# Performance work log

Hardware: AMD Instinct MI355X
Metric: run time of the kernel (lower is better)

Reference implementation:

```python
import jax, jax.numpy as jnp
import numpy as np

B, T, D_IN, N_UNITS, N_OUT = 128, 2048, 256, 512, 64
EPS, GAMMA = 0.01, 0.01


def setup_inputs() -> dict:
    key = jax.random.key(0)
    ks = jax.random.split(key, 5)
    x = jax.random.normal(ks[0], (B, T, D_IN), dtype=jnp.float32)
    # Linear weights ~ N(0, 1/input_dim) per the torch init
    Vh_w = jax.random.normal(ks[1], (N_UNITS, D_IN), dtype=jnp.float32) / D_IN
    Vh_b = jnp.zeros((N_UNITS,), dtype=jnp.float32)
    Vz_w = jax.random.normal(ks[2], (N_UNITS, D_IN), dtype=jnp.float32) / D_IN
    Vz_b = jnp.zeros((N_UNITS,), dtype=jnp.float32)
    # W ~ N(0, init_W_std/input_dim), square [n_units, n_units]
    W = jax.random.normal(ks[3], (N_UNITS, N_UNITS), dtype=jnp.float32) / D_IN
    fc_w = jax.random.normal(ks[4], (N_OUT, N_UNITS), dtype=jnp.float32) * 0.02
    fc_b = jnp.zeros((N_OUT,), dtype=jnp.float32)
    return {"x": x, "Vh_w": Vh_w, "Vh_b": Vh_b, "Vz_w": Vz_w, "Vz_b": Vz_b,
            "W": W, "fc_w": fc_w, "fc_b": fc_b}


def reference(x, Vh_w, Vh_b, Vz_w, Vz_b, W, fc_w, fc_b):
    n_units = W.shape[0]
    # precompute antisymmetric-minus-diffusion matrix once
    A = W - W.T - GAMMA * jnp.eye(n_units, dtype=W.dtype)
    # precompute input projections for all timesteps (batched GEMM)
    vh_x = jnp.einsum('btd,nd->btn', x, Vh_w) + Vh_b  # [B,T,N]
    vz_x = jnp.einsum('btd,nd->btn', x, Vz_w) + Vz_b  # [B,T,N]

    def step(h, inp):
        vh_t, vz_t = inp
        WmWT_h = h @ A                       # [B,N]
        f = jnp.tanh(WmWT_h + vh_t) * jax.nn.sigmoid(WmWT_h + vz_t)
        h = h + EPS * f
        return h, None

    h0 = jnp.zeros((x.shape[0], n_units), dtype=x.dtype)
    # scan over time: inputs shaped [T,B,N]
    hT, _ = jax.lax.scan(step, h0,
                         (jnp.swapaxes(vh_x, 0, 1), jnp.swapaxes(vz_x, 0, 1)))
    return hT @ fc_w.T + fc_b
```

## Files before the change

### kernel.cpp

```cpp
#include <hip/hip_runtime.h>
#include <stdint.h>

#define B_SZ   128
#define T_LEN  2048
#define DIN    256
#define NU     512
#define NOUT   64
#define EPS_F  0.01f
#define GAM_F  0.01f
#define KT     32
#define NTILES (T_LEN / KT)

typedef uint32_t u32;
typedef _Float16 h16;
typedef _Float16 __attribute__((ext_vector_type(2))) h16x2;
typedef _Float16 __attribute__((ext_vector_type(8))) h16x8;
typedef float    __attribute__((ext_vector_type(4))) f32x4;
typedef unsigned int __attribute__((ext_vector_type(4))) u32x4;

#define WS_A    0
#define WS_WH   131072
#define WS_WZ   196608
#define WS_EXCH 262144
#define NQUAD   43

__device__ __forceinline__ u32 pack2(float lo, float hi) {
  h16x2 v; v.x = (h16)lo; v.y = (h16)hi;
  return __builtin_bit_cast(u32, v);
}

__device__ __forceinline__ float fdot2(u32 h2, u32 a2, float acc) {
#if __has_builtin(__builtin_amdgcn_fdot2)
  return __builtin_amdgcn_fdot2(__builtin_bit_cast(h16x2, h2),
                                __builtin_bit_cast(h16x2, a2), acc, false);
#else
  h16x2 hh = __builtin_bit_cast(h16x2, h2);
  h16x2 aa = __builtin_bit_cast(h16x2, a2);
  return acc + (float)hh.x * (float)aa.x + (float)hh.y * (float)aa.y;
#endif
}

__global__ void antirnn_prep(const float* __restrict__ Vh_w,
                             const float* __restrict__ Vz_w,
                             const float* __restrict__ W,
                             u32* __restrict__ ws,
                             float* __restrict__ out) {
  const int idx = blockIdx.x * blockDim.x + threadIdx.x;
  const int stride = gridDim.x * blockDim.x;

  for (int u = idx; u < 131072; u += stride) {
    int e  = u & 3;
    int l  = (u >> 2) & 63;
    int pq = (u >> 8) & 15;
    int c4 = (u >> 12) & 3;
    int w  = (u >> 14) & 3;
    int jh = (u >> 16) & 1;
    int p  = pq * 4 + e;
    int i0 = w * 128 + 2 * p;
    int j  = jh * 256 + l * 4 + c4;
    float lo = W[i0 * NU + j]       - W[j * NU + i0]     - (i0 == j     ? GAM_F : 0.f);
    float hi = W[(i0 + 1) * NU + j] - W[j * NU + i0 + 1] - ((i0 + 1) == j ? GAM_F : 0.f);
    ws[WS_A + u] = pack2(lo, hi);
  }
  for (int u = idx; u < 65536; u += stride) {
    int fl = u * 2;
    ws[WS_WH + u] = pack2(Vh_w[fl], Vh_w[fl + 1]);
    ws[WS_WZ + u] = pack2(Vz_w[fl], Vz_w[fl + 1]);
  }
  for (int u = idx; u < B_SZ * 2 * 2 * NQUAD * 4; u += stride) ws[WS_EXCH + u] = 0;
  for (int u = idx; u < B_SZ * NOUT; u += stride) out[u] = 0.f;
}

__global__ __launch_bounds__(256, 1) void antirnn_scan(
    const float* __restrict__ x,
    const float* __restrict__ vh_b, const float* __restrict__ vz_b,
    const float* __restrict__ fc_w, const float* __restrict__ fc_b,
    u32* __restrict__ ws, float* __restrict__ out) {

  __shared__ h16  xs[32 * 256];
  __shared__ h16  ph[256 * 36];
  __shared__ h16  pz[256 * 36];
  __shared__ float part[4 * 256];
  __shared__ u32  hp[256];

  const int tid = threadIdx.x;
  const int w   = tid >> 6;
  const int l   = tid & 63;
  const int bid = blockIdx.x;
  const int b   = bid & 127;
  const int jh  = bid >> 7;

  u32 a[256];
  {
    const uint4* Ap = reinterpret_cast<const uint4*>(ws + WS_A) + (jh * 4 + w) * 4096 + l;
#pragma unroll
    for (int rq = 0; rq < 64; ++rq) {
      uint4 q = Ap[rq * 64];
      int base = (rq >> 4) * 64 + (rq & 15) * 4;
      a[base + 0] = q.x; a[base + 1] = q.y; a[base + 2] = q.z; a[base + 3] = q.w;
    }
  }

  hp[tid] = 0;

  const float* xrow = x + (long)b * T_LEN * DIN;
  float hreg = 0.f;
  const h16* Wn_h = reinterpret_cast<const h16*>(ws + WS_WH);
  const h16* Wn_z = reinterpret_cast<const h16*>(ws + WS_WZ);
  uint4* exch = reinterpret_cast<uint4*>(ws + WS_EXCH);

  const int  peerHalf   = 1 - jh;
  const bool isPeerWave = ((w >> 1) == peerHalf);
  const int  qbase      = (w & 1) * 21;

#pragma unroll 1
  for (int tile = 0; tile < NTILES; ++tile) {
#pragma unroll
    for (int it = 0; it < 16; ++it) {
      int fp = it * 256 + tid;
      int s  = fp >> 7, dp = fp & 127;
      float2 v = *reinterpret_cast<const float2*>(xrow + (tile * KT + s) * DIN + dp * 2);
      int byteaddr = (s * 512 + dp * 4) ^ ((s & 7) << 4);
      *reinterpret_cast<u32*>(reinterpret_cast<char*>(xs) + byteaddr) = pack2(v.x, v.y);
    }
    __syncthreads();

    {
      f32x4 acch[2][4], accz[2][4];
#pragma unroll
      for (int mt = 0; mt < 2; ++mt)
#pragma unroll
        for (int nt = 0; nt < 4; ++nt) {
          acch[mt][nt] = (f32x4){0.f, 0.f, 0.f, 0.f};
          accz[mt][nt] = (f32x4){0.f, 0.f, 0.f, 0.f};
        }
      const int lk = (l >> 4) * 8;
      const int ln = l & 15;
#pragma unroll
      for (int kk = 0; kk < 8; ++kk) {
        h16x8 af[2];
#pragma unroll
        for (int mt = 0; mt < 2; ++mt) {
          int s = mt * 16 + ln;
          int byteaddr = (s * 512 + kk * 64 + (l >> 4) * 16) ^ ((s & 7) << 4);
          af[mt] = *reinterpret_cast<const h16x8*>(reinterpret_cast<const char*>(xs) + byteaddr);
        }
#pragma unroll
        for (int nt = 0; nt < 4; ++nt) {
          int ng = jh * 256 + w * 64 + nt * 16 + ln;
          h16x8 bh = *reinterpret_cast<const h16x8*>(Wn_h + ng * 256 + kk * 32 + lk);
          h16x8 bz = *reinterpret_cast<const h16x8*>(Wn_z + ng * 256 + kk * 32 + lk);
#pragma unroll
          for (int mt = 0; mt < 2; ++mt) {
            acch[mt][nt] = __builtin_amdgcn_mfma_f32_16x16x32_f16(af[mt], bh, acch[mt][nt], 0, 0, 0);
            accz[mt][nt] = __builtin_amdgcn_mfma_f32_16x16x32_f16(af[mt], bz, accz[mt][nt], 0, 0, 0);
          }
        }
      }
#pragma unroll
      for (int nt = 0; nt < 4; ++nt) {
        int n  = w * 64 + nt * 16 + ln;
        float bh_ = vh_b[jh * 256 + n];
        float bz_ = vz_b[jh * 256 + n];
#pragma unroll
        for (int mt = 0; mt < 2; ++mt) {
          int s0 = mt * 16 + (l >> 4) * 4;
          *reinterpret_cast<u32*>(&ph[n * 36 + s0])     = pack2(acch[mt][nt].x + bh_, acch[mt][nt].y + bh_);
          *reinterpret_cast<u32*>(&ph[n * 36 + s0 + 2]) = pack2(acch[mt][nt].z + bh_, acch[mt][nt].w + bh_);
          *reinterpret_cast<u32*>(&pz[n * 36 + s0])     = pack2(accz[mt][nt].x + bz_, accz[mt][nt].y + bz_);
          *reinterpret_cast<u32*>(&pz[n * 36 + s0 + 2]) = pack2(accz[mt][nt].z + bz_, accz[mt][nt].w + bz_);
        }
      }
    }
    __syncthreads();

#pragma unroll 1
    for (int s = 0; s < KT; ++s) {
      const int t = tile * KT + s;

      if (isPeerWave && t > 0 && l <= 21) {
        int q = qbase + l;
        const uint4* src = exch + (((b * 2 + peerHalf) * 2 + (t & 1)) * NQUAD) + q;
        u32x4 v;
        do {
          asm volatile("global_load_dwordx4 %0, %1, off sc0 sc1\n\ts_waitcnt vmcnt(0)"
                       : "=v"(v) : "v"(src) : "memory");
        } while (v[0] != (u32)t);
#pragma unroll
        for (int k2 = 0; k2 < 3; ++k2) {
          int pi = q * 3 + k2;
          if (pi < 128) hp[peerHalf * 128 + pi] = v[1 + k2];
        }
      }

      u32 hq[64];
      {
        const uint4* hpw = reinterpret_cast<const uint4*>(&hp[w * 64]);
#pragma unroll
        for (int pq = 0; pq < 16; ++pq) {
          uint4 qq = hpw[pq];
          hq[pq * 4 + 0] = qq.x; hq[pq * 4 + 1] = qq.y;
          hq[pq * 4 + 2] = qq.z; hq[pq * 4 + 3] = qq.w;
        }
      }
      float acc0 = 0.f, acc1 = 0.f, acc2 = 0.f, acc3 = 0.f;
#pragma unroll
      for (int p = 0; p < 64; ++p) {
        acc0 = fdot2(hq[p], a[p],        acc0);
        acc1 = fdot2(hq[p], a[64 + p],   acc1);
        acc2 = fdot2(hq[p], a[128 + p],  acc2);
        acc3 = fdot2(hq[p], a[192 + p],  acc3);
      }
      {
        f32x4 pv = {acc0, acc1, acc2, acc3};
        *reinterpret_cast<f32x4*>(&part[w * 256 + l * 4]) = pv;
      }
      __syncthreads();

      {
        float pre = part[tid] + part[256 + tid] + part[512 + tid] + part[768 + tid];
        float uh  = pre + (float)ph[tid * 36 + s];
        float uz  = pre + (float)pz[tid * 36 + s];
        float uhc = fminf(fmaxf(uh, -20.f), 20.f);
        float e2  = __expf(2.f * uhc);
        float th  = 1.f - 2.f / (e2 + 1.f);
        float sg  = 1.f / (1.f + __expf(-uz));
        hreg += EPS_F * th * sg;
        float other = __shfl_xor(hreg, 1, 64);
        if (!(tid & 1)) hp[jh * 128 + (tid >> 1)] = pack2(hreg, other);
      }
      __syncthreads();

      if ((t + 1 < T_LEN) && w == 0 && l < NQUAD) {
        int p0 = l * 3;
        u32 v0 = hp[jh * 128 + p0];
        u32 v1 = (p0 + 1 < 128) ? hp[jh * 128 + p0 + 1] : 0u;
        u32 v2 = (p0 + 2 < 128) ? hp[jh * 128 + p0 + 2] : 0u;
        u32x4 qd; qd[0] = (u32)(t + 1); qd[1] = v0; qd[2] = v1; qd[3] = v2;
        uint4* dst = exch + (((b * 2 + jh) * 2 + ((t + 1) & 1)) * NQUAD) + l;
        asm volatile("global_store_dwordx4 %0, %1, off sc0 sc1"
                     :: "v"(dst), "v"(qd) : "memory");
      }
    }
  }

  __syncthreads();
  part[tid] = hreg;
  __syncthreads();
  if (tid < NOUT) {
    float acc = (jh == 0) ? fc_b[tid] : 0.f;
    const float* fr = fc_w + tid * NU + jh * 256;
#pragma unroll 4
    for (int c = 0; c < 256; ++c) acc += part[c] * fr[c];
    atomicAdd(out + b * NOUT + tid, acc);
  }
}

extern "C" void kernel_launch(void* const* d_in, const int* in_sizes, int n_in,
                              void* d_out, int out_size, void* d_ws, size_t ws_size,
                              hipStream_t stream) {
  const float* x    = (const float*)d_in[0];
  const float* Vh_w = (const float*)d_in[1];
  const float* Vh_b = (const float*)d_in[2];
  const float* Vz_w = (const float*)d_in[3];
  const float* Vz_b = (const float*)d_in[4];
  const float* W    = (const float*)d_in[5];
  const float* fc_w = (const float*)d_in[6];
  const float* fc_b = (const float*)d_in[7];
  float* out = (float*)d_out;
  u32*   ws  = (u32*)d_ws;

  antirnn_prep<<<512, 256, 0, stream>>>(Vh_w, Vz_w, W, ws, out);
  antirnn_scan<<<256, 256, 0, stream>>>(x, Vh_b, Vz_b, fc_w, fc_b, ws, out);
}
```

Baseline: 4.993 ms.

## Interleave two batch chains per block to hide cross-block exchange latency

Each block now handles two batch rows and alternates their recurrence steps, so one chain's peer exchange can be in flight while the other chain computes. Peer h-state for the next chain is prefetched asynchronously into LDS with global_load_lds, and the code falls back to polling only if the flag is stale. The grid drops from 256 to 128 blocks. Per-block serial work doubles and only half the CUs are used, in exchange for hiding the inter-block synchronisation latency that dominates each step.

```diff
diff --git a/kernel.cpp b/kernel.cpp
--- a/kernel.cpp
+++ b/kernel.cpp
@@ -10,6 +10,7 @@
 #define GAM_F  0.01f
 #define KT     32
 #define NTILES (T_LEN / KT)
+#define NC     2
 
 typedef uint32_t u32;
 typedef _Float16 h16;
@@ -17,6 +18,9 @@
 typedef _Float16 __attribute__((ext_vector_type(8))) h16x8;
 typedef float    __attribute__((ext_vector_type(4))) f32x4;
 typedef unsigned int __attribute__((ext_vector_type(4))) u32x4;
+
+typedef const __attribute__((address_space(1))) u32* gas_u32p;
+typedef __attribute__((address_space(3))) u32* las_u32p;
 
 #define WS_A    0
 #define WS_WH   131072
@@ -78,17 +82,19 @@
     u32* __restrict__ ws, float* __restrict__ out) {
 
   __shared__ h16  xs[32 * 256];
-  __shared__ h16  ph[256 * 36];
-  __shared__ h16  pz[256 * 36];
+  __shared__ h16  ph[NC][256 * 36];
+  __shared__ h16  pz[NC][256 * 36];
   __shared__ float part[4 * 256];
-  __shared__ u32  hp[256];
+  __shared__ u32  hp[NC * 256];
+  __shared__ u32x4 stageQ[NC][44];
 
   const int tid = threadIdx.x;
   const int w   = tid >> 6;
   const int l   = tid & 63;
   const int bid = blockIdx.x;
-  const int b   = bid & 127;
-  const int jh  = bid >> 7;
+  const int g   = bid & 63;
+  const int jh  = bid >> 6;
+  const int b0  = g * NC;
 
   u32 a[256];
   {
@@ -101,158 +107,187 @@
     }
   }
 
-  hp[tid] = 0;
-
-  const float* xrow = x + (long)b * T_LEN * DIN;
-  float hreg = 0.f;
+  hp[tid] = 0; hp[256 + tid] = 0;
+
+  float hreg[NC] = {0.f, 0.f};
   const h16* Wn_h = reinterpret_cast<const h16*>(ws + WS_WH);
   const h16* Wn_z = reinterpret_cast<const h16*>(ws + WS_WZ);
   uint4* exch = reinterpret_cast<uint4*>(ws + WS_EXCH);
 
   const int  peerHalf   = 1 - jh;
   const bool isPeerWave = ((w >> 1) == peerHalf);
-  const int  qbase      = (w & 1) * 21;
+  const int  wl         = w & 1;
+  const int  qbase      = wl * 21;
+  const int  sendWave   = jh * 2;
 
 #pragma unroll 1
   for (int tile = 0; tile < NTILES; ++tile) {
-#pragma unroll
-    for (int it = 0; it < 16; ++it) {
-      int fp = it * 256 + tid;
-      int s  = fp >> 7, dp = fp & 127;
-      float2 v = *reinterpret_cast<const float2*>(xrow + (tile * KT + s) * DIN + dp * 2);
-      int byteaddr = (s * 512 + dp * 4) ^ ((s & 7) << 4);
-      *reinterpret_cast<u32*>(reinterpret_cast<char*>(xs) + byteaddr) = pack2(v.x, v.y);
+#pragma unroll 1
+    for (int c = 0; c < NC; ++c) {
+      const float* xrow = x + (long)(b0 + c) * T_LEN * DIN;
+#pragma unroll
+      for (int it = 0; it < 16; ++it) {
+        int fp = it * 256 + tid;
+        int s  = fp >> 7, dp = fp & 127;
+        float2 v = *reinterpret_cast<const float2*>(xrow + (tile * KT + s) * DIN + dp * 2);
+        int byteaddr = (s * 512 + dp * 4) ^ ((s & 7) << 4);
+        *reinterpret_cast<u32*>(reinterpret_cast<char*>(xs) + byteaddr) = pack2(v.x, v.y);
+      }
+      __syncthreads();
+
+      {
+        f32x4 acch[2][4], accz[2][4];
+#pragma unroll
+        for (int mt = 0; mt < 2; ++mt)
+#pragma unroll
+          for (int nt = 0; nt < 4; ++nt) {
+            acch[mt][nt] = (f32x4){0.f, 0.f, 0.f, 0.f};
+            accz[mt][nt] = (f32x4){0.f, 0.f, 0.f, 0.f};
+          }
+        const int lk = (l >> 4) * 8;
+        const int ln = l & 15;
+#pragma unroll
+        for (int kk = 0; kk < 8; ++kk) {
+          h16x8 af[2];
+#pragma unroll
+          for (int mt = 0; mt < 2; ++mt) {
+            int s = mt * 16 + ln;
+            int byteaddr = (s * 512 + kk * 64 + (l >> 4) * 16) ^ ((s & 7) << 4);
+            af[mt] = *reinterpret_cast<const h16x8*>(reinterpret_cast<const char*>(xs) + byteaddr);
+          }
+#pragma unroll
+          for (int nt = 0; nt < 4; ++nt) {
+            int ng = jh * 256 + w * 64 + nt * 16 + ln;
+            h16x8 bh = *reinterpret_cast<const h16x8*>(Wn_h + ng * 256 + kk * 32 + lk);
+            h16x8 bz = *reinterpret_cast<const h16x8*>(Wn_z + ng * 256 + kk * 32 + lk);
+#pragma unroll
+            for (int mt = 0; mt < 2; ++mt) {
+              acch[mt][nt] = __builtin_amdgcn_mfma_f32_16x16x32_f16(af[mt], bh, acch[mt][nt], 0, 0, 0);
+              accz[mt][nt] = __builtin_amdgcn_mfma_f32_16x16x32_f16(af[mt], bz, accz[mt][nt], 0, 0, 0);
+            }
+          }
+        }
+#pragma unroll
+        for (int nt = 0; nt < 4; ++nt) {
+          int n  = w * 64 + nt * 16 + ln;
+          float bh_ = vh_b[jh * 256 + n];
+          float bz_ = vz_b[jh * 256 + n];
+#pragma unroll
+          for (int mt = 0; mt < 2; ++mt) {
+            int s0 = mt * 16 + (l >> 4) * 4;
+            *reinterpret_cast<u32*>(&ph[c][n * 36 + s0])     = pack2(acch[mt][nt].x + bh_, acch[mt][nt].y + bh_);
+            *reinterpret_cast<u32*>(&ph[c][n * 36 + s0 + 2]) = pack2(acch[mt][nt].z + bh_, acch[mt][nt].w + bh_);
+            *reinterpret_cast<u32*>(&pz[c][n * 36 + s0])     = pack2(accz[mt][nt].x + bz_, accz[mt][nt].y + bz_);
+            *reinterpret_cast<u32*>(&pz[c][n * 36 + s0 + 2]) = pack2(accz[mt][nt].z + bz_, accz[mt][nt].w + bz_);
+          }
+        }
+      }
+      __syncthreads();
     }
-    __syncthreads();
-
-    {
-      f32x4 acch[2][4], accz[2][4];
-#pragma unroll
-      for (int mt = 0; mt < 2; ++mt)
-#pragma unroll
-        for (int nt = 0; nt < 4; ++nt) {
-          acch[mt][nt] = (f32x4){0.f, 0.f, 0.f, 0.f};
-          accz[mt][nt] = (f32x4){0.f, 0.f, 0.f, 0.f};
-        }
-      const int lk = (l >> 4) * 8;
-      const int ln = l & 15;
-#pragma unroll
-      for (int kk = 0; kk < 8; ++kk) {
-        h16x8 af[2];
-#pragma unroll
-        for (int mt = 0; mt < 2; ++mt) {
-          int s = mt * 16 + ln;
-          int byteaddr = (s * 512 + kk * 64 + (l >> 4) * 16) ^ ((s & 7) << 4);
-          af[mt] = *reinterpret_cast<const h16x8*>(reinterpret_cast<const char*>(xs) + byteaddr);
-        }
-#pragma unroll
-        for (int nt = 0; nt < 4; ++nt) {
-          int ng = jh * 256 + w * 64 + nt * 16 + ln;
-          h16x8 bh = *reinterpret_cast<const h16x8*>(Wn_h + ng * 256 + kk * 32 + lk);
-          h16x8 bz = *reinterpret_cast<const h16x8*>(Wn_z + ng * 256 + kk * 32 + lk);
-#pragma unroll
-          for (int mt = 0; mt < 2; ++mt) {
-            acch[mt][nt] = __builtin_amdgcn_mfma_f32_16x16x32_f16(af[mt], bh, acch[mt][nt], 0, 0, 0);
-            accz[mt][nt] = __builtin_amdgcn_mfma_f32_16x16x32_f16(af[mt], bz, accz[mt][nt], 0, 0, 0);
-          }
-        }
-      }
-#pragma unroll
-      for (int nt = 0; nt < 4; ++nt) {
-        int n  = w * 64 + nt * 16 + ln;
-        float bh_ = vh_b[jh * 256 + n];
-        float bz_ = vz_b[jh * 256 + n];
-#pragma unroll
-        for (int mt = 0; mt < 2; ++mt) {
-          int s0 = mt * 16 + (l >> 4) * 4;
-          *reinterpret_cast<u32*>(&ph[n * 36 + s0])     = pack2(acch[mt][nt].x + bh_, acch[mt][nt].y + bh_);
-          *reinterpret_cast<u32*>(&ph[n * 36 + s0 + 2]) = pack2(acch[mt][nt].z + bh_, acch[mt][nt].w + bh_);
-          *reinterpret_cast<u32*>(&pz[n * 36 + s0])     = pack2(accz[mt][nt].x + bz_, accz[mt][nt].y + bz_);
-          *reinterpret_cast<u32*>(&pz[n * 36 + s0 + 2]) = pack2(accz[mt][nt].z + bz_, accz[mt][nt].w + bz_);
+
+#pragma unroll 1
+    for (int s = 0; s < KT; ++s) {
+      const int t = tile * KT + s;
+#pragma unroll 1
+      for (int c = 0; c < NC; ++c) {
+        const int cn = 1 - c;
+        const int tn = t + c;
+
+        if (isPeerWave && l <= 21) {
+          const int q = qbase + l;
+          {
+            const uint4* nsrc = exch + ((((b0 + cn) * 2 + peerHalf) * 2 + (tn & 1)) * NQUAD) + q;
+            __builtin_amdgcn_global_load_lds((gas_u32p)(const u32*)nsrc,
+                                             (las_u32p)(u32*)&stageQ[cn][wl * 22],
+                                             16, 0, 0x11 );
+          }
+          if (t > 0) {
+            asm volatile("s_waitcnt vmcnt(1)" ::: "memory");
+            u32x4 v = *reinterpret_cast<const u32x4*>(&stageQ[c][wl * 22 + l]);
+            if (v[0] != (u32)t) {
+              const uint4* src = exch + ((((b0 + c) * 2 + peerHalf) * 2 + (t & 1)) * NQUAD) + q;
+              do {
+                asm volatile("global_load_dwordx4 %0, %1, off sc0 sc1\n\ts_waitcnt vmcnt(0)"
+                             : "=v"(v) : "v"(src) : "memory");
+              } while (v[0] != (u32)t);
+            }
+            const int lo = wl * 64, hiEx = lo + 64;
+#pragma unroll
+            for (int k2 = 0; k2 < 3; ++k2) {
+              int pi = q * 3 + k2;
+              if (pi >= lo && pi < hiEx) hp[c * 256 + peerHalf * 128 + pi] = v[1 + k2];
+            }
+          }
+        }
+
+        float acc0 = 0.f, acc1 = 0.f, acc2 = 0.f, acc3 = 0.f;
+        {
+          const uint4* hpw = reinterpret_cast<const uint4*>(&hp[c * 256 + w * 64]);
+#pragma unroll
+          for (int gq = 0; gq < 4; ++gq) {
+            u32 hq[16];
+#pragma unroll
+            for (int pq = 0; pq < 4; ++pq) {
+              uint4 qq = hpw[gq * 4 + pq];
+              hq[pq * 4 + 0] = qq.x; hq[pq * 4 + 1] = qq.y;
+              hq[pq * 4 + 2] = qq.z; hq[pq * 4 + 3] = qq.w;
+            }
+#pragma unroll
+            for (int p = 0; p < 16; ++p) {
+              int pp = gq * 16 + p;
+              acc0 = fdot2(hq[p], a[pp],        acc0);
+              acc1 = fdot2(hq[p], a[64 + pp],   acc1);
+              acc2 = fdot2(hq[p], a[128 + pp],  acc2);
+              acc3 = fdot2(hq[p], a[192 + pp],  acc3);
+            }
+          }
+        }
+        {
+          f32x4 pv = {acc0, acc1, acc2, acc3};
+          *reinterpret_cast<f32x4*>(&part[w * 256 + l * 4]) = pv;
+        }
+        __syncthreads();
+
+        {
+          float pre = part[tid] + part[256 + tid] + part[512 + tid] + part[768 + tid];
+          float uh  = pre + (float)ph[c][tid * 36 + s];
+          float uz  = pre + (float)pz[c][tid * 36 + s];
+          float uhc = fminf(fmaxf(uh, -20.f), 20.f);
+          float e2  = __expf(2.f * uhc);
+          float th  = 1.f - 2.f / (e2 + 1.f);
+          float sg  = 1.f / (1.f + __expf(-uz));
+          hreg[c] += EPS_F * th * sg;
+          float other = __shfl_xor(hreg[c], 1, 64);
+          if (!(tid & 1)) hp[c * 256 + jh * 128 + (tid >> 1)] = pack2(hreg[c], other);
+        }
+        __syncthreads();
+
+        if ((t + 1 < T_LEN) && w == sendWave && l < NQUAD) {
+          int p0 = l * 3;
+          u32 v0 = hp[c * 256 + jh * 128 + p0];
+          u32 v1 = (p0 + 1 < 128) ? hp[c * 256 + jh * 128 + p0 + 1] : 0u;
+          u32 v2 = (p0 + 2 < 128) ? hp[c * 256 + jh * 128 + p0 + 2] : 0u;
+          u32x4 qd; qd[0] = (u32)(t + 1); qd[1] = v0; qd[2] = v1; qd[3] = v2;
+          uint4* dst = exch + ((((b0 + c) * 2 + jh) * 2 + ((t + 1) & 1)) * NQUAD) + l;
+          asm volatile("global_store_dwordx4 %0, %1, off sc0 sc1"
+                       :: "v"(dst), "v"(qd) : "memory");
         }
       }
     }
+  }
+
+#pragma unroll 1
+  for (int c = 0; c < NC; ++c) {
     __syncthreads();
-
-#pragma unroll 1
-    for (int s = 0; s < KT; ++s) {
-      const int t = tile * KT + s;
-
-      if (isPeerWave && t > 0 && l <= 21) {
-        int q = qbase + l;
-        const uint4* src = exch + (((b * 2 + peerHalf) * 2 + (t & 1)) * NQUAD) + q;
-        u32x4 v;
-        do {
-          asm volatile("global_load_dwordx4 %0, %1, off sc0 sc1\n\ts_waitcnt vmcnt(0)"
-                       : "=v"(v) : "v"(src) : "memory");
-        } while (v[0] != (u32)t);
-#pragma unroll
-        for (int k2 = 0; k2 < 3; ++k2) {
-          int pi = q * 3 + k2;
-          if (pi < 128) hp[peerHalf * 128 + pi] = v[1 + k2];
-        }
-      }
-
-      u32 hq[64];
-      {
-        const uint4* hpw = reinterpret_cast<const uint4*>(&hp[w * 64]);
-#pragma unroll
-        for (int pq = 0; pq < 16; ++pq) {
-          uint4 qq = hpw[pq];
-          hq[pq * 4 + 0] = qq.x; hq[pq * 4 + 1] = qq.y;
-          hq[pq * 4 + 2] = qq.z; hq[pq * 4 + 3] = qq.w;
-        }
-      }
-      float acc0 = 0.f, acc1 = 0.f, acc2 = 0.f, acc3 = 0.f;
-#pragma unroll
-      for (int p = 0; p < 64; ++p) {
-        acc0 = fdot2(hq[p], a[p],        acc0);
-        acc1 = fdot2(hq[p], a[64 + p],   acc1);
-        acc2 = fdot2(hq[p], a[128 + p],  acc2);
-        acc3 = fdot2(hq[p], a[192 + p],  acc3);
-      }
-      {
-        f32x4 pv = {acc0, acc1, acc2, acc3};
-        *reinterpret_cast<f32x4*>(&part[w * 256 + l * 4]) = pv;
-      }
-      __syncthreads();
-
-      {
-        float pre = part[tid] + part[256 + tid] + part[512 + tid] + part[768 + tid];
-        float uh  = pre + (float)ph[tid * 36 + s];
-        float uz  = pre + (float)pz[tid * 36 + s];
-        float uhc = fminf(fmaxf(uh, -20.f), 20.f);
-        float e2  = __expf(2.f * uhc);
-        float th  = 1.f - 2.f / (e2 + 1.f);
-        float sg  = 1.f / (1.f + __expf(-uz));
-        hreg += EPS_F * th * sg;
-        float other = __shfl_xor(hreg, 1, 64);
-        if (!(tid & 1)) hp[jh * 128 + (tid >> 1)] = pack2(hreg, other);
-      }
-      __syncthreads();
-
-      if ((t + 1 < T_LEN) && w == 0 && l < NQUAD) {
-        int p0 = l * 3;
-        u32 v0 = hp[jh * 128 + p0];
-        u32 v1 = (p0 + 1 < 128) ? hp[jh * 128 + p0 + 1] : 0u;
-        u32 v2 = (p0 + 2 < 128) ? hp[jh * 128 + p0 + 2] : 0u;
-        u32x4 qd; qd[0] = (u32)(t + 1); qd[1] = v0; qd[2] = v1; qd[3] = v2;
-        uint4* dst = exch + (((b * 2 + jh) * 2 + ((t + 1) & 1)) * NQUAD) + l;
-        asm volatile("global_store_dwordx4 %0, %1, off sc0 sc1"
-                     :: "v"(dst), "v"(qd) : "memory");
-      }
+    part[tid] = hreg[c];
+    __syncthreads();
+    if (tid < NOUT) {
+      float acc = (jh == 0) ? fc_b[tid] : 0.f;
+      const float* fr = fc_w + tid * NU + jh * 256;
+#pragma unroll 4
+      for (int cc = 0; cc < 256; ++cc) acc += part[cc] * fr[cc];
+      atomicAdd(out + (b0 + c) * NOUT + tid, acc);
     }
-  }
-
-  __syncthreads();
-  part[tid] = hreg;
-  __syncthreads();
-  if (tid < NOUT) {
-    float acc = (jh == 0) ? fc_b[tid] : 0.f;
-    const float* fr = fc_w + tid * NU + jh * 256;
-#pragma unroll 4
-    for (int c = 0; c < 256; ++c) acc += part[c] * fr[c];
-    atomicAdd(out + b * NOUT + tid, acc);
   }
 }
 
@@ -271,5 +306,5 @@
   u32*   ws  = (u32*)d_ws;
 
   antirnn_prep<<<512, 256, 0, stream>>>(Vh_w, Vz_w, W, ws, out);
-  antirnn_scan<<<256, 256, 0, stream>>>(x, Vh_b, Vz_b, fc_w, fc_b, ws, out);
-}
+  antirnn_scan<<<128, 256, 0, stream>>>(x, Vh_b, Vz_b, fc_w, fc_b, ws, out);
+}
```

Result: slower. 10.46 ms (+109.5%).
